# Performance work log

Hardware: AMD Instinct MI355X
Metric: run time of the kernel (lower is better)

## Reference

```python
import jax, jax.numpy as jnp
import numpy as np

N, E = 50000, 500000
SD, VD, HID, DEPTH = 128, 3, 64, 4
CUTOFF = 5.0


def setup_inputs() -> dict:
    key = jax.random.key(0)
    ks = jax.random.split(key, 13)
    s = jax.random.normal(ks[0], (N, SD), jnp.float32)
    v = jax.random.normal(ks[1], (N, VD, 3), jnp.float32)
    edge_index = jax.random.randint(ks[2], (2, E), 0, N, jnp.int32)
    d = jax.random.uniform(ks[3], (E, 1), jnp.float32) * CUTOFF  # distances within cutoff
    r = jax.random.normal(ks[4], (E, 3), jnp.float32)            # relative position vectors

    def lin(k, shp):
        return jax.random.normal(k, shp, jnp.float32) * (1.0 / np.sqrt(shp[-2]))

    # per-layer stacked parameters [DEPTH, ...]
    W1 = lin(ks[5], (DEPTH, 2 * SD + 1, HID)); b1 = jnp.zeros((DEPTH, HID), jnp.float32)
    W2 = lin(ks[6], (DEPTH, HID, HID));        b2 = jnp.zeros((DEPTH, HID), jnp.float32)
    W3 = lin(ks[7], (DEPTH, HID, SD + 2 * VD)); b3 = jnp.zeros((DEPTH, SD + 2 * VD), jnp.float32)
    Wn1 = lin(ks[8], (DEPTH, 2 * SD, HID)); bn1 = jnp.zeros((DEPTH, HID), jnp.float32)
    Wn2 = lin(ks[9], (DEPTH, HID, SD));     bn2 = jnp.zeros((DEPTH, SD), jnp.float32)
    return dict(s=s, v=v, edge_index=edge_index, d=d, r=r,
                W1=W1, b1=b1, W2=W2, b2=b2, W3=W3, b3=b3,
                Wn1=Wn1, bn1=bn1, Wn2=Wn2, bn2=bn2)


def _egnn(s, v, edge_index, d, r, W1, b1, W2, b2, W3, b3, Wn1, bn1, Wn2, bn2):
    dst, src = edge_index[0], edge_index[1]
    # cosine cutoff envelope, zero beyond CUTOFF
    C = 0.5 * (jnp.cos(jnp.pi * d / CUTOFF) + 1.0) * (d < CUTOFF)  # [E,1]
    # in-degree counts for 'mean' vector aggregation (fixed, layer-independent)
    cnt = jax.ops.segment_sum(jnp.ones((E,), jnp.float32), dst, num_segments=N)
    inv_cnt = 1.0 / jnp.maximum(cnt, 1.0)  # [N]
    for l in range(DEPTH):
        # gather + edge MLP (EGCL message)
        h = jnp.concatenate([s[dst], s[src], d], axis=-1)      # [E, 2*SD+1]
        h = jax.nn.silu(h @ W1[l] + b1[l])
        h = jax.nn.silu(h @ W2[l] + b2[l])
        m = h @ W3[l] + b3[l]                                   # [E, SD+2*VD]
        ms, gv, gr = m[:, :SD], m[:, SD:SD + VD], m[:, SD + VD:]
        ms = ms * C                                             # scalar message
        # equivariant vector message: gated source vectors + gated edge direction
        vm = (v[src] * gv[:, :, None] + r[:, None, :] * gr[:, :, None]) * C[:, :, None]
        # scatter aggregate: sum for scalars, mean for vectors (vector_aggr='mean')
        s_agg = jax.ops.segment_sum(ms, dst, num_segments=N)    # [N, SD]
        v_agg = jax.ops.segment_sum(vm, dst, num_segments=N) * inv_cnt[:, None, None]
        # node update (residual)
        u = jax.nn.silu(jnp.concatenate([s, s_agg], axis=-1) @ Wn1[l] + bn1[l])
        s = s + u @ Wn2[l] + bn2[l]
        v = v + v_agg
    return s, v


def reference(s, v, edge_index, d, r, W1, b1, W2, b2, W3, b3, Wn1, bn1, Wn2, bn2):
    return _egnn(s, v, edge_index, d, r, W1, b1, W2, b2, W3, b3, Wn1, bn1, Wn2, bn2)
```

## Files before the change

kernel.cpp:

```cpp
#include <hip/hip_runtime.h>
#include <hip/hip_bf16.h>
#include <math.h>

#define N_NODES 50000
#define N_EDGES 500000
#define SD 128
#define VD 3
#define HID 64
#define DEPTH 4

#define NF1 32
#define NF2 8
#define NF3 18
#define W1F_SH (NF1 * 512)
#define W2F_SH (NF2 * 512)
#define W3F_SH (NF3 * 512)
#define WPK_SH (W1F_SH + W2F_SH + W3F_SH)

#define WN1T_SH (64 * 256)
#define WN2T_SH (128 * 64)
#define WN_SH (WN1T_SH + WN2T_SH)

#define EDGE_GRID 512
#define NTILES (N_EDGES / 16)
#define EDGE_ITERS ((NTILES + EDGE_GRID * 4 - 1) / (EDGE_GRID * 4))

typedef __attribute__((ext_vector_type(8))) short short8;
typedef __attribute__((ext_vector_type(4))) float f32x4;

__device__ __forceinline__ float silu_f(float x) {
    return x / (1.0f + __expf(-x));
}

__device__ __forceinline__ unsigned short f2bf(float x) {
    __hip_bfloat16 h = __float2bfloat16(x);
    return *reinterpret_cast<unsigned short*>(&h);
}

__device__ __forceinline__ float bf2f(unsigned short u) {
    union { unsigned int i; float f; } c; c.i = ((unsigned int)u) << 16;
    return c.f;
}

__device__ __forceinline__ short8 cvt8(const float* __restrict__ p) {
    short8 o;
    #pragma unroll
    for (int i = 0; i < 8; i++) o[i] = (short)f2bf(p[i]);
    return o;
}

__device__ __forceinline__ void wavefence() { __builtin_amdgcn_wave_barrier(); }


__global__ void cast_s_kernel(const float* __restrict__ in, float* __restrict__ out,
                              unsigned short* __restrict__ out_bf, int n) {
    int i = blockIdx.x * blockDim.x + threadIdx.x;
    if (i < n) { float x = in[i]; out[i] = x; out_bf[i] = f2bf(x); }
}

__global__ void copy_kernel(const float* __restrict__ in, float* __restrict__ out, int n) {
    int i = blockIdx.x * blockDim.x + threadIdx.x;
    if (i < n) out[i] = in[i];
}

__global__ void prep_edges(const int* __restrict__ ei, const float* __restrict__ d,
                           float* __restrict__ C, int* __restrict__ cnti) {
    int e = blockIdx.x * blockDim.x + threadIdx.x;
    if (e >= N_EDGES) return;
    float de = d[e];
    float c = 0.5f * (cosf(3.14159265358979323846f * de * (1.0f / 5.0f)) + 1.0f);
    C[e] = (de < 5.0f) ? c : 0.0f;
    atomicAdd(&cnti[ei[e]], 1);
}

__global__ void inv_cnt_kernel(const int* __restrict__ cnti, float* __restrict__ inv_cnt) {
    int i = blockIdx.x * blockDim.x + threadIdx.x;
    if (i < N_NODES) inv_cnt[i] = 1.0f / fmaxf((float)cnti[i], 1.0f);
}

__global__ __launch_bounds__(1024) void scan_block(const int* __restrict__ cnti,
                                                   int* __restrict__ offs,
                                                   int* __restrict__ bsum) {
    __shared__ int sh[1024];
    int tid = threadIdx.x;
    int idx = blockIdx.x * 1024 + tid;
    int x = (idx < N_NODES) ? cnti[idx] : 0;
    sh[tid] = x;
    __syncthreads();
    for (int off = 1; off < 1024; off <<= 1) {
        int y = (tid >= off) ? sh[tid - off] : 0;
        __syncthreads();
        sh[tid] += y;
        __syncthreads();
    }
    if (idx < N_NODES) offs[idx] = sh[tid] - x;
    if (tid == 1023) bsum[blockIdx.x] = sh[1023];
}

__global__ void scan_partials(int* __restrict__ bsum, int nb, int* __restrict__ offs_total) {
    if (threadIdx.x == 0 && blockIdx.x == 0) {
        int acc = 0;
        for (int i = 0; i < nb; i++) { int t = bsum[i]; bsum[i] = acc; acc += t; }
        offs_total[0] = acc;
    }
}

__global__ __launch_bounds__(1024) void scan_apply(int* __restrict__ offs,
                                                   const int* __restrict__ bsum) {
    int idx = blockIdx.x * 1024 + threadIdx.x;
    if (idx < N_NODES) offs[idx] += bsum[blockIdx.x];
}

__global__ void build_perm(const int* __restrict__ ei, const int* __restrict__ offs,
                           int* __restrict__ cursor, int* __restrict__ eids) {
    int e = blockIdx.x * blockDim.x + threadIdx.x;
    if (e >= N_EDGES) return;
    int dst = ei[e];
    int p = offs[dst] + atomicAdd(&cursor[dst], 1);
    eids[p] = e;
}

__global__ void permute_edges(const int* __restrict__ ei, const float* __restrict__ d,
                              const float* __restrict__ C, const float* __restrict__ r,
                              const int* __restrict__ eids,
                              int* __restrict__ dst_s, int* __restrict__ src_s,
                              float* __restrict__ d_s, float* __restrict__ C_s,
                              float* __restrict__ r_s) {
    int p = blockIdx.x * blockDim.x + threadIdx.x;
    if (p >= N_EDGES) return;
    int e = eids[p];
    dst_s[p] = ei[e];
    src_s[p] = ei[N_EDGES + e];
    d_s[p] = d[e];
    C_s[p] = C[e];
    r_s[3 * (size_t)p + 0] = r[3 * (size_t)e + 0];
    r_s[3 * (size_t)p + 1] = r[3 * (size_t)e + 1];
    r_s[3 * (size_t)p + 2] = r[3 * (size_t)e + 2];
}

__global__ void prep_weights(const float* __restrict__ W1, const float* __restrict__ W2,
                             const float* __restrict__ W3, unsigned short* __restrict__ Wpk) {
    int idx = blockIdx.x * blockDim.x + threadIdx.x;
    if (idx >= DEPTH * WPK_SH) return;
    int l = idx / WPK_SH;
    int j = idx - l * WPK_SH;
    float val = 0.0f;
    if (j < W1F_SH) {
        int f = j >> 9, rrr = j & 511;
        int lane = rrr >> 3, jj = rrr & 7;
        int q = lane >> 4, lo = lane & 15;
        int ks = f >> 2, t = f & 3;
        int k = ks * 32 + q * 8 + jj;
        int n = t * 16 + lo;
        val = W1[((size_t)l * 257 + k) * 64 + n];
    } else if (j < W1F_SH + W2F_SH) {
        int jj2 = j - W1F_SH;
        int f = jj2 >> 9, rrr = jj2 & 511;
        int lane = rrr >> 3, jj = rrr & 7;
        int q = lane >> 4, lo = lane & 15;
        int ks = f >> 2, t = f & 3;
        int k = ks * 32 + q * 8 + jj;
        int n = t * 16 + lo;
        val = W2[((size_t)l * 64 + k) * 64 + n];
    } else {
        int jj3 = j - W1F_SH - W2F_SH;
        int f = jj3 >> 9, rrr = jj3 & 511;
        int lane = rrr >> 3, jj = rrr & 7;
        int q = lane >> 4, lo = lane & 15;
        int ks = f / 9, t = f - ks * 9;
        int k = ks * 32 + q * 8 + jj;
        int n = t * 16 + lo;
        val = (n < 134) ? W3[((size_t)l * 64 + k) * 134 + n] : 0.0f;
    }
    Wpk[idx] = f2bf(val);
}

__global__ void prep_node_weights(const float* __restrict__ Wn1, const float* __restrict__ Wn2,
                                  unsigned short* __restrict__ Wnpk) {
    int idx = blockIdx.x * blockDim.x + threadIdx.x;
    if (idx >= DEPTH * WN_SH) return;
    int l = idx / WN_SH;
    int j = idx - l * WN_SH;
    float val;
    if (j < WN1T_SH) {
        int n = j / 256, k = j - n * 256;
        val = Wn1[((size_t)l * 256 + k) * 64 + n];
    } else {
        int jj = j - WN1T_SH;
        int n = jj / 64, k = jj - n * 64;
        val = Wn2[((size_t)l * 64 + k) * 128 + n];
    }
    Wnpk[idx] = f2bf(val);
}

__global__ __launch_bounds__(256, 2) void edge_mfma(
    const unsigned short* __restrict__ s_bf, const float* __restrict__ v,
    const int* __restrict__ dst_s, const int* __restrict__ src_s,
    const float* __restrict__ d_s, const float* __restrict__ C_s,
    const float* __restrict__ r_s,
    const unsigned short* __restrict__ Wpk_l,
    const float* __restrict__ W1r,
    const float* __restrict__ b1, const float* __restrict__ b2,
    const float* __restrict__ b3,
    float* __restrict__ s_agg, float* __restrict__ v_agg)
{
    __shared__ __align__(16) unsigned short w1f[W1F_SH];
    __shared__ __align__(16) unsigned short w3f[W3F_SH];
    __shared__ __align__(16) unsigned short Hb[4][16 * 72];
    __shared__ float gb[4][16][6];
    __shared__ float vtile[4][16][9];
    __shared__ int tdst[4][16];

    const int tid  = threadIdx.x;
    const int wl   = tid >> 6;
    const int lane = tid & 63;
    const int lo   = lane & 15;
    const int q    = lane >> 4;

    {
        const short8* g1 = reinterpret_cast<const short8*>(Wpk_l);
        const short8* g3 = reinterpret_cast<const short8*>(Wpk_l + W1F_SH + W2F_SH);
        short8* l1 = reinterpret_cast<short8*>(w1f);
        short8* l3 = reinterpret_cast<short8*>(w3f);
        for (int i = tid; i < W1F_SH / 8; i += 256) l1[i] = g1[i];
        for (int i = tid; i < W3F_SH / 8; i += 256) l3[i] = g3[i];
    }
    __syncthreads();

    const unsigned short* w2g = Wpk_l + W1F_SH;

    float bb1[4], wr1[4], bb2[4], bb3[9];
    #pragma unroll
    for (int t = 0; t < 4; t++) { bb1[t] = b1[t * 16 + lo]; wr1[t] = W1r[t * 16 + lo]; }
    #pragma unroll
    for (int t = 0; t < 4; t++) bb2[t] = b2[t * 16 + lo];
    #pragma unroll
    for (int t = 0; t < 9; t++) { int n = t * 16 + lo; bb3[t] = (n < 134) ? b3[n] : 0.0f; }

    int raw0 = blockIdx.x * 4 + wl;
    bool val_c = true;
    long eb = (long)raw0 * 16;
    int dn_c;
    short8 ad[4], asf[4];
    float4 dd4, ce4;
    float vsr[9], rv[3], cel_t = 0.0f;
    {
        dn_c = dst_s[eb + lo];
        int sn = src_s[eb + lo];
        dd4 = *reinterpret_cast<const float4*>(d_s + eb + 4 * q);
        ce4 = *reinterpret_cast<const float4*>(C_s + eb + 4 * q);
        const unsigned short* rd = s_bf + (size_t)dn_c * SD;
        const unsigned short* rs = s_bf + (size_t)sn * SD;
        #pragma unroll
        for (int ks = 0; ks < 4; ks++) {
            ad[ks]  = *reinterpret_cast<const short8*>(rd + ks * 32 + q * 8);
            asf[ks] = *reinterpret_cast<const short8*>(rs + ks * 32 + q * 8);
        }
        if (lane < 16) {
            cel_t = C_s[eb + lane];
            #pragma unroll
            for (int t = 0; t < 9; t++) vsr[t] = v[(size_t)sn * 9 + t];
            #pragma unroll
            for (int t = 0; t < 3; t++) rv[t] = r_s[3 * eb + 3 * lane + t];
        }
    }

    for (int it = 0; it < EDGE_ITERS; it++) {
        int raw_n = (it + 1) * (EDGE_GRID * 4) + blockIdx.x * 4 + wl;
        bool val_n = (raw_n < NTILES);
        int tile_n = val_n ? raw_n : (NTILES - 1);
        long ebn = (long)tile_n * 16;
        int dn_n = dst_s[ebn + lo];
        int sn_n = src_s[ebn + lo];
        float4 dd4_n = *reinterpret_cast<const float4*>(d_s + ebn + 4 * q);
        float4 ce4_n = *reinterpret_cast<const float4*>(C_s + ebn + 4 * q);
        float cel_n = 0.0f, rv_n[3];
        if (lane < 16) {
            cel_n = C_s[ebn + lane];
            #pragma unroll
            for (int t = 0; t < 3; t++) rv_n[t] = r_s[3 * ebn + 3 * lane + t];
        }

        f32x4 acc1[4];
        #pragma unroll
        for (int t = 0; t < 4; t++) {
            float dd[4] = { dd4.x, dd4.y, dd4.z, dd4.w };
            #pragma unroll
            for (int rr = 0; rr < 4; rr++) acc1[t][rr] = bb1[t] + dd[rr] * wr1[t];
        }
        #pragma unroll
        for (int ks = 0; ks < 4; ks++) {
            #pragma unroll
            for (int t = 0; t < 4; t++) {
                short8 b = *reinterpret_cast<const short8*>(&w1f[((ks * 4 + t) * 64 + lane) * 8]);
                acc1[t] = __builtin_amdgcn_mfma_f32_16x16x32_bf16(ad[ks], b, acc1[t], 0, 0, 0);
            }
        }
        #pragma unroll
        for (int ks = 0; ks < 4; ks++) {
            #pragma unroll
            for (int t = 0; t < 4; t++) {
                short8 b = *reinterpret_cast<const short8*>(&w1f[(((ks + 4) * 4 + t) * 64 + lane) * 8]);
                acc1[t] = __builtin_amdgcn_mfma_f32_16x16x32_bf16(asf[ks], b, acc1[t], 0, 0, 0);
            }
        }
        #pragma unroll
        for (int t = 0; t < 4; t++)
            #pragma unroll
            for (int rr = 0; rr < 4; rr++)
                Hb[wl][(4 * q + rr) * 72 + t * 16 + lo] = f2bf(silu_f(acc1[t][rr]));
        wavefence();

        short8 a2[2];
        #pragma unroll
        for (int ks = 0; ks < 2; ks++)
            a2[ks] = *reinterpret_cast<const short8*>(&Hb[wl][lo * 72 + ks * 32 + q * 8]);
        f32x4 acc2[4];
        #pragma unroll
        for (int t = 0; t < 4; t++) {
            #pragma unroll
            for (int rr = 0; rr < 4; rr++) acc2[t][rr] = bb2[t];
        }
        #pragma unroll
        for (int ks = 0; ks < 2; ks++) {
            #pragma unroll
            for (int t = 0; t < 4; t++) {
                short8 b = *reinterpret_cast<const short8*>(w2g + ((ks * 4 + t) * 64 + lane) * 8);
                acc2[t] = __builtin_amdgcn_mfma_f32_16x16x32_bf16(a2[ks], b, acc2[t], 0, 0, 0);
            }
        }

        short8 ad_n[4], as_n[4];
        {
            const unsigned short* rd = s_bf + (size_t)dn_n * SD;
            const unsigned short* rs = s_bf + (size_t)sn_n * SD;
            #pragma unroll
            for (int ks = 0; ks < 4; ks++) {
                ad_n[ks] = *reinterpret_cast<const short8*>(rd + ks * 32 + q * 8);
                as_n[ks] = *reinterpret_cast<const short8*>(rs + ks * 32 + q * 8);
            }
        }
        float vsr_n[9];
        if (lane < 16) {
            #pragma unroll
            for (int t = 0; t < 9; t++) vsr_n[t] = v[(size_t)sn_n * 9 + t];
        }

        wavefence();
        #pragma unroll
        for (int t = 0; t < 4; t++)
            #pragma unroll
            for (int rr = 0; rr < 4; rr++)
                Hb[wl][(4 * q + rr) * 72 + t * 16 + lo] = f2bf(silu_f(acc2[t][rr]));
        wavefence();

        short8 a3[2];
        #pragma unroll
        for (int ks = 0; ks < 2; ks++)
            a3[ks] = *reinterpret_cast<const short8*>(&Hb[wl][lo * 72 + ks * 32 + q * 8]);
        f32x4 acc3[9];
        #pragma unroll
        for (int t = 0; t < 9; t++) {
            #pragma unroll
            for (int rr = 0; rr < 4; rr++) acc3[t][rr] = bb3[t];
        }
        #pragma unroll
        for (int ks = 0; ks < 2; ks++) {
            #pragma unroll
            for (int t = 0; t < 9; t++) {
                short8 b = *reinterpret_cast<const short8*>(&w3f[((ks * 9 + t) * 64 + lane) * 8]);
                acc3[t] = __builtin_amdgcn_mfma_f32_16x16x32_bf16(a3[ks], b, acc3[t], 0, 0, 0);
            }
        }

        if (lo < 6) {
            #pragma unroll
            for (int rr = 0; rr < 4; rr++) gb[wl][4 * q + rr][lo] = acc3[8][rr];
        }
        if (lane < 16) tdst[wl][lane] = dn_c;
        wavefence();

        if (lane < 16) {
            #pragma unroll
            for (int vi = 0; vi < VD; vi++) {
                float gv = gb[wl][lane][vi], gr = gb[wl][lane][VD + vi];
                vtile[wl][lane][vi * 3 + 0] = (vsr[vi * 3 + 0] * gv + rv[0] * gr) * cel_t;
                vtile[wl][lane][vi * 3 + 1] = (vsr[vi * 3 + 1] * gv + rv[1] * gr) * cel_t;
                vtile[wl][lane][vi * 3 + 2] = (vsr[vi * 3 + 2] * gv + rv[2] * gr) * cel_t;
            }
        }
        wavefence();

        if (val_c) {
            float ce[4] = { ce4.x, ce4.y, ce4.z, ce4.w };
            int sseg = 0;
            while (sseg < 16) {
                int dnode = tdst[wl][sseg];
                int eseg = sseg + 1;
                while (eseg < 16 && tdst[wl][eseg] == dnode) eseg++;
                float* srow = s_agg + (size_t)dnode * SD;
                #pragma unroll
                for (int t = 0; t < 8; t++) {
                    float p = 0.0f;
                    #pragma unroll
                    for (int rr = 0; rr < 4; rr++) {
                        int row = 4 * q + rr;
                        p += (row >= sseg && row < eseg) ? acc3[t][rr] * ce[rr] : 0.0f;
                    }
                    p += __shfl_xor(p, 16);
                    p += __shfl_xor(p, 32);
                    if (q == 0) atomicAdd(&srow[t * 16 + lo], p);
                }
                if (lane < 9) {
                    float pv = 0.0f;
                    for (int i = sseg; i < eseg; i++) pv += vtile[wl][i][lane];
                    atomicAdd(&v_agg[(size_t)dnode * 9 + lane], pv);
                }
                sseg = eseg;
            }
        }

        val_c = val_n;
        eb = ebn;
        dn_c = dn_n;
        dd4 = dd4_n; ce4 = ce4_n;
        cel_t = cel_n;
        #pragma unroll
        for (int ks = 0; ks < 4; ks++) { ad[ks] = ad_n[ks]; asf[ks] = as_n[ks]; }
        #pragma unroll
        for (int t = 0; t < 9; t++) vsr[t] = vsr_n[t];
        #pragma unroll
        for (int t = 0; t < 3; t++) rv[t] = rv_n[t];
    }
}

__global__ __launch_bounds__(256) void node_mfma(
    float* __restrict__ s, float* __restrict__ v, unsigned short* __restrict__ s_bf,
    const float* __restrict__ s_agg, const float* __restrict__ v_agg,
    const float* __restrict__ inv_cnt,
    const unsigned short* __restrict__ Wn_l,
    const float* __restrict__ bn1, const float* __restrict__ bn2)
{
    __shared__ __align__(16) unsigned short Hb[4][16 * 72];

    const int tid  = threadIdx.x;
    const int wl   = tid >> 6;
    const int lane = tid & 63;
    const int lo   = lane & 15;
    const int q    = lane >> 4;
    const int nb   = blockIdx.x * 64 + wl * 16;

    int na = nb + lo; if (na > N_NODES - 1) na = N_NODES - 1;
    const unsigned short* rs = s_bf  + (size_t)na * SD;
    const float*          ra = s_agg + (size_t)na * SD;

    f32x4 acc1[4];
    #pragma unroll
    for (int t = 0; t < 4; t++) {
        float bb = bn1[t * 16 + lo];
        #pragma unroll
        for (int rr = 0; rr < 4; rr++) acc1[t][rr] = bb;
    }
    #pragma unroll
    for (int ks = 0; ks < 4; ks++) {
        short8 a = *reinterpret_cast<const short8*>(rs + ks * 32 + q * 8);
        #pragma unroll
        for (int t = 0; t < 4; t++) {
            short8 b = *reinterpret_cast<const short8*>(Wn_l + (t * 16 + lo) * 256 + ks * 32 + q * 8);
            acc1[t] = __builtin_amdgcn_mfma_f32_16x16x32_bf16(a, b, acc1[t], 0, 0, 0);
        }
    }
    #pragma unroll
    for (int ks = 0; ks < 4; ks++) {
        short8 a = cvt8(ra + ks * 32 + q * 8);
        #pragma unroll
        for (int t = 0; t < 4; t++) {
            short8 b = *reinterpret_cast<const short8*>(Wn_l + (t * 16 + lo) * 256 + 128 + ks * 32 + q * 8);
            acc1[t] = __builtin_amdgcn_mfma_f32_16x16x32_bf16(a, b, acc1[t], 0, 0, 0);
        }
    }
    #pragma unroll
    for (int t = 0; t < 4; t++)
        #pragma unroll
        for (int rr = 0; rr < 4; rr++)
            Hb[wl][(4 * q + rr) * 72 + t * 16 + lo] = f2bf(silu_f(acc1[t][rr]));
    wavefence();

    const unsigned short* w2g = Wn_l + WN1T_SH;
    f32x4 acc2[8];
    #pragma unroll
    for (int t = 0; t < 8; t++) {
        float bb = bn2[t * 16 + lo];
        #pragma unroll
        for (int rr = 0; rr < 4; rr++) acc2[t][rr] = bb;
    }
    #pragma unroll
    for (int ks = 0; ks < 2; ks++) {
        short8 a = *reinterpret_cast<const short8*>(&Hb[wl][lo * 72 + ks * 32 + q * 8]);
        #pragma unroll
        for (int t = 0; t < 8; t++) {
            short8 b = *reinterpret_cast<const short8*>(w2g + (t * 16 + lo) * 64 + ks * 32 + q * 8);
            acc2[t] = __builtin_amdgcn_mfma_f32_16x16x32_bf16(a, b, acc2[t], 0, 0, 0);
        }
    }

    #pragma unroll
    for (int t = 0; t < 8; t++) {
        int col = t * 16 + lo;
        #pragma unroll
        for (int rr = 0; rr < 4; rr++) {
            int node = nb + 4 * q + rr;
            if (node < N_NODES) {
                size_t idx = (size_t)node * SD + col;
                float ns = s[idx] + acc2[t][rr];
                s[idx] = ns;
                s_bf[idx] = f2bf(ns);
            }
        }
    }

    if (lane < 16) {
        int node = nb + lane;
        if (node < N_NODES) {
            float ic = inv_cnt[node];
            #pragma unroll
            for (int t = 0; t < VD * 3; t++)
                v[(size_t)node * 9 + t] += v_agg[(size_t)node * 9 + t] * ic;
        }
    }
}

extern "C" void kernel_launch(void* const* d_in, const int* in_sizes, int n_in,
                              void* d_out, int out_size, void* d_ws, size_t ws_size,
                              hipStream_t stream)
{
    (void)in_sizes; (void)n_in; (void)out_size; (void)ws_size;
    const float* s_in = (const float*)d_in[0];
    const float* v_in = (const float*)d_in[1];
    const int*   ei   = (const int*)d_in[2];
    const float* d_e  = (const float*)d_in[3];
    const float* r_e  = (const float*)d_in[4];
    const float* W1   = (const float*)d_in[5];
    const float* b1   = (const float*)d_in[6];
    const float* W2   = (const float*)d_in[7];
    const float* b2   = (const float*)d_in[8];
    const float* W3   = (const float*)d_in[9];
    const float* b3   = (const float*)d_in[10];
    const float* Wn1  = (const float*)d_in[11];
    const float* bn1  = (const float*)d_in[12];
    const float* Wn2  = (const float*)d_in[13];
    const float* bn2  = (const float*)d_in[14];

    float* s = (float*)d_out;
    float* v = s + (size_t)N_NODES * SD;

    float* ws      = (float*)d_ws;
    float* s_agg   = ws;
    float* v_agg   = s_agg + (size_t)N_NODES * SD;
    float* cntinv  = v_agg + (size_t)N_NODES * 9;
    float* Cbuf    = cntinv + N_NODES;
    int*   cnti    = (int*)(Cbuf + N_EDGES);
    int*   offs    = cnti + N_NODES;
    int*   cursor  = offs + N_NODES + 1;
    int*   eids    = cursor + N_NODES;
    int*   bsum    = eids + N_EDGES;
    int*   dst_s   = bsum + 64;
    int*   src_s   = dst_s + N_EDGES;
    float* d_s     = (float*)(src_s + N_EDGES);
    float* C_s     = d_s + N_EDGES;
    float* r_s     = C_s + N_EDGES;
    uintptr_t up   = (uintptr_t)(r_s + (size_t)3 * N_EDGES);
    up = (up + 15) & ~(uintptr_t)15;
    unsigned short* s_bf = (unsigned short*)up;
    unsigned short* Wpk  = s_bf + (size_t)N_NODES * SD;
    unsigned short* Wnpk = Wpk + (size_t)DEPTH * WPK_SH;

    hipMemsetAsync(cnti, 0, sizeof(int) * (size_t)N_NODES, stream);
    hipMemsetAsync(cursor, 0, sizeof(int) * (size_t)N_NODES, stream);

    cast_s_kernel<<<(N_NODES * SD + 255) / 256, 256, 0, stream>>>(s_in, s, s_bf, N_NODES * SD);
    copy_kernel<<<(N_NODES * VD * 3 + 255) / 256, 256, 0, stream>>>(v_in, v, N_NODES * VD * 3);
    prep_edges<<<(N_EDGES + 255) / 256, 256, 0, stream>>>(ei, d_e, Cbuf, cnti);
    inv_cnt_kernel<<<(N_NODES + 255) / 256, 256, 0, stream>>>(cnti, cntinv);

    const int NB = (N_NODES + 1023) / 1024;
    scan_block<<<NB, 1024, 0, stream>>>(cnti, offs, bsum);
    scan_partials<<<1, 64, 0, stream>>>(bsum, NB, offs + N_NODES);
    scan_apply<<<NB, 1024, 0, stream>>>(offs, bsum);
    build_perm<<<(N_EDGES + 255) / 256, 256, 0, stream>>>(ei, offs, cursor, eids);
    permute_edges<<<(N_EDGES + 255) / 256, 256, 0, stream>>>(
        ei, d_e, Cbuf, r_e, eids, dst_s, src_s, d_s, C_s, r_s);

    prep_weights<<<(DEPTH * WPK_SH + 255) / 256, 256, 0, stream>>>(W1, W2, W3, Wpk);
    prep_node_weights<<<(DEPTH * WN_SH + 255) / 256, 256, 0, stream>>>(Wn1, Wn2, Wnpk);

    for (int l = 0; l < DEPTH; l++) {
        hipMemsetAsync(s_agg, 0, sizeof(float) * (size_t)N_NODES * (SD + 9), stream);
        edge_mfma<<<EDGE_GRID, 256, 0, stream>>>(
            s_bf, v, dst_s, src_s, d_s, C_s, r_s,
            Wpk + (size_t)l * WPK_SH,
            W1 + ((size_t)l * 257 + 256) * 64,
            b1 + (size_t)l * HID, b2 + (size_t)l * HID, b3 + (size_t)l * (SD + 2 * VD),
            s_agg, v_agg);
        node_mfma<<<(N_NODES + 63) / 64, 256, 0, stream>>>(
            s, v, s_bf, s_agg, v_agg, cntinv,
            Wnpk + (size_t)l * WN_SH,
            bn1 + (size_t)l * HID, bn2 + (size_t)l * SD);
    }
}
```

Baseline: 1.007 ms.

## Raise edge kernel occupancy by streaming W3 from global and ballot-based segmenting

Removes the W3 fragment copy from shared memory and reads it directly from global/L2, cutting LDS use so three blocks per CU fit, and grows the edge grid to match. The per-destination segment detection moves from an LDS table and scalar loop to a wavefront ballot over destination changes. The cutoff scaling is applied once to the accumulators instead of inside each segment, and the vector tile is loaded into registers once. The risk is extra global/L2 traffic for W3 and higher register pressure under the tighter launch bound.

After: 1.684 ms. 1.67x slower.

```diff
diff --git a/kernel.cpp b/kernel.cpp
--- a/kernel.cpp
+++ b/kernel.cpp
@@ -21,7 +21,7 @@
 #define WN2T_SH (128 * 64)
 #define WN_SH (WN1T_SH + WN2T_SH)
 
-#define EDGE_GRID 512
+#define EDGE_GRID 768
 #define NTILES (N_EDGES / 16)
 #define EDGE_ITERS ((NTILES + EDGE_GRID * 4 - 1) / (EDGE_GRID * 4))
 
@@ -193,7 +193,7 @@
     Wnpk[idx] = f2bf(val);
 }
 
-__global__ __launch_bounds__(256, 2) void edge_mfma(
+__global__ __launch_bounds__(256, 3) void edge_mfma(
     const unsigned short* __restrict__ s_bf, const float* __restrict__ v,
     const int* __restrict__ dst_s, const int* __restrict__ src_s,
     const float* __restrict__ d_s, const float* __restrict__ C_s,
@@ -205,11 +205,9 @@
     float* __restrict__ s_agg, float* __restrict__ v_agg)
 {
     __shared__ __align__(16) unsigned short w1f[W1F_SH];
-    __shared__ __align__(16) unsigned short w3f[W3F_SH];
     __shared__ __align__(16) unsigned short Hb[4][16 * 72];
     __shared__ float gb[4][16][6];
     __shared__ float vtile[4][16][9];
-    __shared__ int tdst[4][16];
 
     const int tid  = threadIdx.x;
     const int wl   = tid >> 6;
@@ -219,15 +217,13 @@
 
     {
         const short8* g1 = reinterpret_cast<const short8*>(Wpk_l);
-        const short8* g3 = reinterpret_cast<const short8*>(Wpk_l + W1F_SH + W2F_SH);
         short8* l1 = reinterpret_cast<short8*>(w1f);
-        short8* l3 = reinterpret_cast<short8*>(w3f);
         for (int i = tid; i < W1F_SH / 8; i += 256) l1[i] = g1[i];
-        for (int i = tid; i < W3F_SH / 8; i += 256) l3[i] = g3[i];
     }
     __syncthreads();
 
     const unsigned short* w2g = Wpk_l + W1F_SH;
+    const unsigned short* w3g = Wpk_l + W1F_SH + W2F_SH;
 
     float bb1[4], wr1[4], bb2[4], bb3[9];
     #pragma unroll
@@ -368,7 +364,7 @@
         for (int ks = 0; ks < 2; ks++) {
             #pragma unroll
             for (int t = 0; t < 9; t++) {
-                short8 b = *reinterpret_cast<const short8*>(&w3f[((ks * 9 + t) * 64 + lane) * 8]);
+                short8 b = *reinterpret_cast<const short8*>(w3g + ((ks * 9 + t) * 64 + lane) * 8);
                 acc3[t] = __builtin_amdgcn_mfma_f32_16x16x32_bf16(a3[ks], b, acc3[t], 0, 0, 0);
             }
         }
@@ -377,7 +373,6 @@
             #pragma unroll
             for (int rr = 0; rr < 4; rr++) gb[wl][4 * q + rr][lo] = acc3[8][rr];
         }
-        if (lane < 16) tdst[wl][lane] = dn_c;
         wavefence();
 
         if (lane < 16) {
@@ -392,12 +387,24 @@
         wavefence();
 
         if (val_c) {
-            float ce[4] = { ce4.x, ce4.y, ce4.z, ce4.w };
-            int sseg = 0;
-            while (sseg < 16) {
-                int dnode = tdst[wl][sseg];
-                int eseg = sseg + 1;
-                while (eseg < 16 && tdst[wl][eseg] == dnode) eseg++;
+            #pragma unroll
+            for (int t = 0; t < 8; t++) {
+                acc3[t][0] *= ce4.x; acc3[t][1] *= ce4.y;
+                acc3[t][2] *= ce4.z; acc3[t][3] *= ce4.w;
+            }
+            float vt[16];
+            if (lane < 9) {
+                #pragma unroll
+                for (int i = 0; i < 16; i++) vt[i] = vtile[wl][i][lane];
+            }
+            int prev = __shfl(dn_c, (lane + 63) & 63);
+            unsigned long long bal = __ballot((lo == 0) || (dn_c != prev));
+            unsigned int m = (unsigned int)(bal & 0xffffu);
+            while (m) {
+                int sseg = __builtin_ctz(m);
+                m &= m - 1;
+                int eseg = m ? __builtin_ctz(m) : 16;
+                int dnode = __shfl(dn_c, sseg);
                 float* srow = s_agg + (size_t)dnode * SD;
                 #pragma unroll
                 for (int t = 0; t < 8; t++) {
@@ -405,7 +412,7 @@
                     #pragma unroll
                     for (int rr = 0; rr < 4; rr++) {
                         int row = 4 * q + rr;
-                        p += (row >= sseg && row < eseg) ? acc3[t][rr] * ce[rr] : 0.0f;
+                        p += (row >= sseg && row < eseg) ? acc3[t][rr] : 0.0f;
                     }
                     p += __shfl_xor(p, 16);
                     p += __shfl_xor(p, 32);
@@ -413,10 +420,11 @@
                 }
                 if (lane < 9) {
                     float pv = 0.0f;
-                    for (int i = sseg; i < eseg; i++) pv += vtile[wl][i][lane];
+                    #pragma unroll
+                    for (int i = 0; i < 16; i++)
+                        pv += (i >= sseg && i < eseg) ? vt[i] : 0.0f;
                     atomicAdd(&v_agg[(size_t)dnode * 9 + lane], pv);
                 }
-                sseg = eseg;
             }
         }
 
```
